# Optimization experiments

Hardware: AMD Instinct MI355X
Metric: run time of the kernel (lower is better)

## Reference

```python
import jax, jax.numpy as jnp
import numpy as np

# Production-scale dims (see shape_source)
B = 8            # batch size
P = 32768        # points per sample
Q = 2048         # supernodes per sample
N = B * P        # 262144 total points
S = B * Q        # 16384 total supernodes
MAX_DEG = 32
E = S * MAX_DEG  # 524288 edges
IN_DIM = 16
H = 192          # hidden_dim, divisible by ndim=3, per-dim 64 (even) -> no padding
NDIM = 3
MAX_WAVELENGTH = 10000.0


def sincos_embed(pos):
    # ContinuousSincosEmbed: dim split evenly over ndim, sin/cos halves per coord
    dpn = H // NDIM                                                   # 64
    omega = 1.0 / MAX_WAVELENGTH ** (jnp.arange(0, dpn, 2, dtype=jnp.float32) / dpn)  # [dpn/2]
    out = pos[..., None] * omega                                      # [N, ndim, dpn/2]
    emb = jnp.concatenate([jnp.sin(out), jnp.cos(out)], axis=-1)      # [N, ndim, dpn]
    return emb.reshape(pos.shape[0], H)                               # [N, H]


def setup_inputs() -> dict:
    key = jax.random.key(0)
    ks = jax.random.split(key, 8)
    input_feat = jax.random.normal(ks[0], (N, IN_DIM), jnp.float32)
    input_pos = jax.random.uniform(ks[1], (N, NDIM), jnp.float32) * 100.0
    batch_idx = jnp.repeat(jnp.arange(B, dtype=jnp.int32), P)
    # Q supernodes per sample, globally sorted & unique (as from radius_graph filter)
    ar = jnp.arange(S, dtype=jnp.int32)
    supernode_idxs = (ar // Q) * P + (ar % Q)
    # edges: each supernode is dst of MAX_DEG edges; src within same sample
    dst_idx = jnp.repeat(supernode_idxs, MAX_DEG)
    src_idx = (dst_idx // P) * P + jax.random.randint(ks[2], (E,), 0, P, dtype=jnp.int32)
    # params (LinearProjection = affine)
    W_in = jax.random.normal(ks[3], (IN_DIM, H), jnp.float32) / np.sqrt(IN_DIM)
    b_in = jnp.zeros((H,), jnp.float32)
    W1 = jax.random.normal(ks[4], (2 * H, H), jnp.float32) / np.sqrt(2 * H)
    b1 = jnp.zeros((H,), jnp.float32)
    W2 = jax.random.normal(ks[5], (H, H), jnp.float32) / np.sqrt(H)
    b2 = jnp.zeros((H,), jnp.float32)
    return {"input_feat": input_feat, "input_pos": input_pos,
            "supernode_idxs": supernode_idxs, "batch_idx": batch_idx,
            "src_idx": src_idx, "dst_idx": dst_idx,
            "W_in": W_in, "b_in": b_in, "W1": W1, "b1": b1, "W2": W2, "b2": b2}


def reference(input_feat, input_pos, supernode_idxs, batch_idx, src_idx, dst_idx,
              W_in, b_in, W1, b1, W2, b2):
    # x = input_proj(feat) + pos_embed(pos)        [N, H]
    x = input_feat @ W_in + b_in + sincos_embed(input_pos)
    # gather src/dst node features per edge, concat  [E, 2H]
    m = jnp.concatenate([x[src_idx], x[dst_idx]], axis=1)
    # message MLP: Linear -> GELU(exact) -> Linear   [E, H]
    m = jax.nn.gelu(m @ W1 + b1, approximate=False) @ W2 + b2
    # segment-mean by destination supernode (segment_csr 'mean' equivalent)
    seg = jnp.searchsorted(supernode_idxs, dst_idx)  # [E] in [0, S)
    sums = jax.ops.segment_sum(m, seg, num_segments=S)
    cnt = jax.ops.segment_sum(jnp.ones((E,), m.dtype), seg, num_segments=S)
    pooled = sums / cnt[:, None]                     # [S, H]
    return pooled.reshape(B, S // B, H)              # [B, Q, H]
```

## Files before the change

### kernel.cpp

```cpp
#include <hip/hip_runtime.h>
#include <hip/hip_bf16.h>


#define HD 192
#define INF 16
#define N_NODES 262144
#define N_SUP 16384
#define ROWB 384
#define EP_TILES 4

typedef __attribute__((ext_vector_type(8))) short bf16x8;
typedef __attribute__((ext_vector_type(4))) float f32x4;

__device__ __forceinline__ unsigned f2bf(float f) {
    unsigned x = __float_as_uint(f);
    return (x + 0x7fffu + ((x >> 16) & 1u)) >> 16;
}
__device__ __forceinline__ float bf2f(unsigned short u) {
    return __uint_as_float(((unsigned)u) << 16);
}
__device__ __forceinline__ void gload16(const void* g, void* l) {
    __builtin_amdgcn_global_load_lds(
        (const __attribute__((address_space(1))) unsigned int*)g,
        (__attribute__((address_space(3))) unsigned int*)l, 16, 0, 0);
}
__device__ __forceinline__ void gelu_acc(float v, float& acc) {
    const float m   = v * fmaf(v * v, -0.1029392f, -2.3021178f);
    const float den = 1.f + exp2f(m);
    const float r   = __builtin_amdgcn_rcpf(den);
    acc = fmaf(v, r, acc);
}

__global__ void prep_kernel(const float* __restrict__ W1,
                            const float* __restrict__ Win,
                            unsigned short* __restrict__ Wt,
                            unsigned short* __restrict__ Wb,
                            float* __restrict__ Wint)
{
    const int i = blockIdx.x * 256 + threadIdx.x;
    if (i < 36864) {
        const int n = i / HD, k = i % HD;
        Wt[i] = (unsigned short)f2bf(W1[k * HD + n]);
    } else if (i < 73728) {
        const int j = i - 36864;
        const int n = j / HD, k = j % HD;
        Wb[j] = (unsigned short)f2bf(W1[(size_t)(HD + k) * HD + n]);
    } else if (i < 76800) {
        const int j = i - 73728;
        const int c = j / INF, k = j % INF;
        Wint[j] = Win[k * HD + c];
    }
}

__global__ __launch_bounds__(256, 2)
void xcomp_kernel(const float* __restrict__ feat,
                  const float* __restrict__ pos,
                  const float* __restrict__ Wint,
                  const float* __restrict__ bin,
                  unsigned short* __restrict__ xswz)
{
    __shared__ __align__(16) float feat_s[4][256];
    __shared__ float pos_s[4][48];
    __shared__ __align__(16) unsigned short dstg[4][16 * HD];

    const int t = threadIdx.x, w = t >> 6, l = t & 63;

    float win[3][INF];
    #pragma unroll
    for (int d = 0; d < 3; ++d)
        #pragma unroll
        for (int q = 0; q < 4; ++q)
            *reinterpret_cast<float4*>(&win[d][q * 4]) =
                *reinterpret_cast<const float4*>(Wint + (size_t)(l + 64 * d) * INF + q * 4);
    float bcol[3];
    #pragma unroll
    for (int d = 0; d < 3; ++d) bcol[d] = bin[l + 64 * d];
    const float om = exp2f(-(float)(l & 31) * 0.41524101186098287f);
    const float phase = (l < 32) ? 0.f : 1.57079632679f;

    for (int gg = 0; gg < 4; ++gg) {
        const int row0 = blockIdx.x * 256 + gg * 64 + w * 16;

        {
            const float4 f4 = *reinterpret_cast<const float4*>(
                feat + (size_t)(row0 + (l >> 2)) * INF + (l & 3) * 4);
            *reinterpret_cast<float4*>(&feat_s[w][(l >> 2) * 16 + (l & 3) * 4]) = f4;
            if (l < 48) pos_s[w][l] = pos[(size_t)row0 * 3 + l];
        }

        for (int r = 0; r < 16; ++r) {
            float fr[INF];
            #pragma unroll
            for (int q = 0; q < 4; ++q)
                *reinterpret_cast<float4*>(&fr[q * 4]) =
                    *reinterpret_cast<const float4*>(&feat_s[w][r * 16 + q * 4]);
            #pragma unroll
            for (int d = 0; d < 3; ++d) {
                const float pe = __sinf(fmaf(pos_s[w][r * 3 + d], om, phase));
                float acc = bcol[d] + pe;
                #pragma unroll
                for (int k = 0; k < INF; ++k) acc = fmaf(fr[k], win[d][k], acc);
                dstg[w][r * HD + l + 64 * d] = (unsigned short)f2bf(acc);
            }
        }

        #pragma unroll
        for (int q = 0; q < 6; ++q) {
            const int id = q * 64 + l;
            const int rl = id / 24, c = id % 24;
            const bf16x8 v = *reinterpret_cast<const bf16x8*>(&dstg[w][rl * HD + c * 8]);
            *reinterpret_cast<bf16x8*>((char*)xswz +
                (size_t)(row0 + rl) * ROWB + ((c ^ (rl & 7)) * 16)) = v;
        }
    }
}

template<bool GATHER>
__global__ __launch_bounds__(256, 2)
void agemm_kernel(const unsigned short* __restrict__ xswz,
                  const int* __restrict__ gidx,
                  const unsigned short* __restrict__ Wt,
                  const float* __restrict__ bias,
                  unsigned short* __restrict__ outp,
                  const int out_stride,
                  const int ntiles)
{
    __shared__ __align__(16) unsigned short xbuf[2][64 * HD];
    __shared__ int nid[64];

    const int t = threadIdx.x, w = t >> 6, l = t & 63;

    bf16x8 bfr[3][6];
    #pragma unroll
    for (int ct = 0; ct < 3; ++ct) {
        const int col = w * 48 + ct * 16 + (l & 15);
        const unsigned short* wp = Wt + (size_t)col * HD + (l >> 4) * 8;
        #pragma unroll
        for (int ks = 0; ks < 6; ++ks)
            bfr[ct][ks] = *reinterpret_cast<const bf16x8*>(wp + ks * 32);
    }
    float bias_c[3] = {0.f, 0.f, 0.f};
    if (GATHER) {
        #pragma unroll
        for (int ct = 0; ct < 3; ++ct) bias_c[ct] = bias[w * 48 + ct * 16 + (l & 15)];
        if (t < 64) nid[t] = gidx[blockIdx.x * 64 + t];
        __syncthreads();
    }

    auto STAGE = [&](int tile, int buf) {
        char* lbase = (char*)&xbuf[buf][0];
        if constexpr (GATHER) {
            #pragma unroll
            for (int i = 0; i < 6; ++i) {
                const int slot = w * 64 + i * 256 + l;
                const int r = slot / 24, p = slot % 24;
                const int node = nid[r];
                const char* src = (const char*)xswz + (size_t)node * ROWB +
                                  (((p ^ (r & 7)) ^ (node & 7)) * 16);
                gload16(src, lbase + w * 1024 + i * 4096);
            }
        } else {
            const char* gb = (const char*)xswz +
                             (size_t)(blockIdx.x * ntiles + tile) * 64 * ROWB;
            #pragma unroll
            for (int i = 0; i < 6; ++i)
                gload16(gb + w * 1024 + i * 4096 + l * 16, lbase + w * 1024 + i * 4096);
        }
    };

    STAGE(0, 0);
    __syncthreads();

    for (int tt = 0; tt < ntiles; ++tt) {
        const int cur = tt & 1;
        if (tt + 1 < ntiles) STAGE(tt + 1, cur ^ 1);

        f32x4 acc[4][3];
        #pragma unroll
        for (int rt = 0; rt < 4; ++rt)
            #pragma unroll
            for (int ct = 0; ct < 3; ++ct)
                acc[rt][ct] = (f32x4){0.f, 0.f, 0.f, 0.f};

        const char* xb = (const char*)&xbuf[cur][0];
        #pragma unroll
        for (int ks = 0; ks < 6; ++ks) {
            bf16x8 af[4];
            #pragma unroll
            for (int rt = 0; rt < 4; ++rt) {
                const int row = rt * 16 + (l & 15);
                const int p = (ks * 4 + (l >> 4)) ^ (l & 7);
                af[rt] = *reinterpret_cast<const bf16x8*>(xb + row * ROWB + p * 16);
            }
            #pragma unroll
            for (int rt = 0; rt < 4; ++rt)
                #pragma unroll
                for (int ct = 0; ct < 3; ++ct)
                    acc[rt][ct] = __builtin_amdgcn_mfma_f32_16x16x32_bf16(
                        af[rt], bfr[ct][ks], acc[rt][ct], 0, 0, 0);
        }
        __syncthreads();

        char* db = (char*)&xbuf[cur][0];
        #pragma unroll
        for (int rt = 0; rt < 4; ++rt)
            #pragma unroll
            for (int ct = 0; ct < 3; ++ct) {
                const int col = w * 48 + ct * 16 + (l & 15);
                const int ch = col >> 3, off = col & 7;
                #pragma unroll
                for (int j = 0; j < 4; ++j) {
                    const int row = rt * 16 + (l >> 4) * 4 + j;
                    *reinterpret_cast<unsigned short*>(
                        db + row * ROWB + ((ch ^ (row & 7)) * 16) + off * 2) =
                        (unsigned short)f2bf(acc[rt][ct][j] + bias_c[ct]);
                }
            }
        const size_t orow0 = GATHER ? (size_t)blockIdx.x * 64
                                    : (size_t)(blockIdx.x * ntiles + tt) * 64;
        #pragma unroll
        for (int q = 0; q < 6; ++q) {
            const int id = q * 64 + l;
            const int rid = id / 6, cc = id % 6;
            const int c = w * 6 + cc;
            const bf16x8 v = *reinterpret_cast<const bf16x8*>(
                db + rid * ROWB + ((c ^ (rid & 7)) * 16));
            *reinterpret_cast<bf16x8*>(outp + (orow0 + rid) * out_stride + c * 8) = v;
        }
        __syncthreads();
    }
}

__global__ __launch_bounds__(256, 2)
void edgepool_kernel(const unsigned short* __restrict__ xswz,
                     const int* __restrict__ src_idx,
                     const unsigned short* __restrict__ Wt,
                     const unsigned short* __restrict__ bC,
                     float* __restrict__ g)
{
    __shared__ __align__(16) unsigned short xbuf[2][64 * HD];

    const int t = threadIdx.x, w = t >> 6, l = t & 63;

    bf16x8 bfr[3][6];
    #pragma unroll
    for (int ct = 0; ct < 3; ++ct) {
        const int col = w * 48 + ct * 16 + (l & 15);
        const unsigned short* wp = Wt + (size_t)col * HD + (l >> 4) * 8;
        #pragma unroll
        for (int ks = 0; ks < 6; ++ks)
            bfr[ct][ks] = *reinterpret_cast<const bf16x8*>(wp + ks * 32);
    }

    auto STAGE = [&](int tile, int buf) {
        char* lbase = (char*)&xbuf[buf][0] + w * 1024;
        const int* se = src_idx + (size_t)(blockIdx.x * EP_TILES + tile) * 64;
        #pragma unroll
        for (int i = 0; i < 6; ++i) {
            const int slot = w * 64 + i * 256 + l;
            const int r = slot / 24, p = slot % 24;
            const int node = se[r];
            const char* src = (const char*)xswz + (size_t)node * ROWB +
                              (((p ^ (r & 7)) ^ (node & 7)) * 16);
            gload16(src, lbase + i * 4096);
        }
    };

    STAGE(0, 0);
    __syncthreads();

    for (int tt = 0; tt < EP_TILES; ++tt) {
        const int cur = tt & 1;
        if (tt + 1 < EP_TILES) STAGE(tt + 1, cur ^ 1);

        f32x4 acc[4][3];
        #pragma unroll
        for (int rt = 0; rt < 4; ++rt)
            #pragma unroll
            for (int ct = 0; ct < 3; ++ct)
                acc[rt][ct] = (f32x4){0.f, 0.f, 0.f, 0.f};

        const char* xb = (const char*)&xbuf[cur][0];
        #pragma unroll
        for (int ks = 0; ks < 6; ++ks) {
            bf16x8 af[4];
            #pragma unroll
            for (int rt = 0; rt < 4; ++rt) {
                const int row = rt * 16 + (l & 15);
                const int p = (ks * 4 + (l >> 4)) ^ (l & 7);
                af[rt] = *reinterpret_cast<const bf16x8*>(xb + row * ROWB + p * 16);
            }
            #pragma unroll
            for (int rt = 0; rt < 4; ++rt)
                #pragma unroll
                for (int ct = 0; ct < 3; ++ct)
                    acc[rt][ct] = __builtin_amdgcn_mfma_f32_16x16x32_bf16(
                        af[rt], bfr[ct][ks], acc[rt][ct], 0, 0, 0);
        }

        const size_t s0 = (size_t)(blockIdx.x * EP_TILES + tt) * 2;
        float bval[2][3];
        #pragma unroll
        for (int sn = 0; sn < 2; ++sn)
            #pragma unroll
            for (int ct = 0; ct < 3; ++ct)
                bval[sn][ct] = bf2f(bC[(s0 + sn) * 384 + w * 48 + ct * 16 + (l & 15)]);

        __syncthreads();

        #pragma unroll
        for (int sn = 0; sn < 2; ++sn)
            #pragma unroll
            for (int ct = 0; ct < 3; ++ct) {
                float part = 0.f;
                #pragma unroll
                for (int rr = 0; rr < 2; ++rr)
                    #pragma unroll
                    for (int j = 0; j < 4; ++j)
                        gelu_acc(acc[sn * 2 + rr][ct][j] + bval[sn][ct], part);
                part += __shfl_xor(part, 16);
                part += __shfl_xor(part, 32);
                if (l < 16)
                    g[(s0 + sn) * HD + w * 48 + ct * 16 + l] = part * 0.03125f;
            }
    }
}

__global__ __launch_bounds__(256, 2)
void gemm192_kernel(const float* __restrict__ A,
                    const float* __restrict__ W,
                    const float* __restrict__ bias,
                    float* __restrict__ out)
{
    __shared__ float xsf[64][196];
    __shared__ float wchunk[32][HD];
    const int t    = threadIdx.x;
    const int row0 = blockIdx.x * 64;

    const float4* ap = reinterpret_cast<const float4*>(A + (size_t)row0 * HD);
    #pragma unroll
    for (int q = 0; q < 12; ++q) {
        const int f4 = t + q * 256;
        const int r = f4 / 48, c = f4 % 48;
        *reinterpret_cast<float4*>(&xsf[r][c * 4]) = ap[f4];
    }

    const int tr = t >> 4;
    const int tc = t & 15;
    float acc[4][12];
    #pragma unroll
    for (int i = 0; i < 4; ++i)
        #pragma unroll
        for (int j = 0; j < 12; ++j) acc[i][j] = 0.f;

    for (int kc = 0; kc < 6; ++kc) {
        __syncthreads();
        {
            const float4* wp = reinterpret_cast<const float4*>(W + kc * 32 * HD);
            float4* wsp = reinterpret_cast<float4*>(&wchunk[0][0]);
            #pragma unroll
            for (int q = 0; q < 6; ++q) wsp[t + q * 256] = wp[t + q * 256];
        }
        __syncthreads();
        #pragma unroll 4
        for (int k = 0; k < 32; ++k) {
            const int kg = kc * 32 + k;
            float xv[4];
            #pragma unroll
            for (int i = 0; i < 4; ++i) xv[i] = xsf[tr * 4 + i][kg];
            float wv[12];
            #pragma unroll
            for (int j4 = 0; j4 < 3; ++j4)
                *reinterpret_cast<float4*>(&wv[j4 * 4]) =
                    *reinterpret_cast<const float4*>(&wchunk[k][tc * 12 + j4 * 4]);
            #pragma unroll
            for (int i = 0; i < 4; ++i)
                #pragma unroll
                for (int j = 0; j < 12; ++j)
                    acc[i][j] = fmaf(xv[i], wv[j], acc[i][j]);
        }
    }

    float bb[12];
    #pragma unroll
    for (int j = 0; j < 12; ++j) bb[j] = bias[tc * 12 + j];

    #pragma unroll
    for (int i = 0; i < 4; ++i) {
        float* o = out + (size_t)(row0 + tr * 4 + i) * HD + tc * 12;
        #pragma unroll
        for (int j4 = 0; j4 < 3; ++j4) {
            float4 v;
            v.x = acc[i][j4 * 4 + 0] + bb[j4 * 4 + 0];
            v.y = acc[i][j4 * 4 + 1] + bb[j4 * 4 + 1];
            v.z = acc[i][j4 * 4 + 2] + bb[j4 * 4 + 2];
            v.w = acc[i][j4 * 4 + 3] + bb[j4 * 4 + 3];
            *reinterpret_cast<float4*>(o + j4 * 4) = v;
        }
    }
}

extern "C" void kernel_launch(void* const* d_in, const int* in_sizes, int n_in,
                              void* d_out, int out_size, void* d_ws, size_t ws_size,
                              hipStream_t stream)
{
    const float* feat = (const float*)d_in[0];
    const float* pos  = (const float*)d_in[1];
    const int*   sup  = (const int*)d_in[2];
    const int*   src  = (const int*)d_in[4];
    const float* Win  = (const float*)d_in[6];
    const float* bin  = (const float*)d_in[7];
    const float* W1   = (const float*)d_in[8];
    const float* b1   = (const float*)d_in[9];
    const float* W2   = (const float*)d_in[10];
    const float* b2   = (const float*)d_in[11];

    char* ws = (char*)d_ws;
    unsigned short* Wt   = (unsigned short*)ws;
    unsigned short* Wb   = (unsigned short*)(ws + 73728);
    float*          Wint = (float*)(ws + 147456);
    unsigned short* x    = (unsigned short*)(ws + 159744);
    char*           C    = ws + 159744 + 100663296;
    float* out = (float*)d_out;

    prep_kernel<<<300, 256, 0, stream>>>(W1, Win, Wt, Wb, Wint);
    xcomp_kernel<<<N_NODES / 256, 256, 0, stream>>>(feat, pos, Wint, bin, x);
    agemm_kernel<true><<<N_SUP / 64, 256, 0, stream>>>(
        x, sup, Wb, b1, (unsigned short*)C, 384, 1);
    edgepool_kernel<<<N_SUP / (2 * EP_TILES), 256, 0, stream>>>(
        x, src, Wt, (const unsigned short*)C, (float*)C);
    gemm192_kernel<<<N_SUP / 64, 256, 0, stream>>>((const float*)C, W2, b2, out);
}
```

Measured before the change: 248.9 us.

## Triple-buffer edge gather pipeline with explicit vmcnt waits and prefetched indices

The edgepool kernel moves to a three-stage LDS ring with prefetch distance two. It replaces __syncthreads with s_waitcnt vmcnt plus s_barrier, doubles tiles per block, and preloads src indices and bias rows into shared memory so tile loops avoid global index loads. The xcomp kernel software-prefetches the next group's feat/pos into registers and raises its occupancy hint. This should hide gather latency better, at the cost of more LDS per block, fewer blocks in the edge kernel, and fragile hand-counted vmcnt values.

```diff
diff --git a/kernel.cpp b/kernel.cpp
--- a/kernel.cpp
+++ b/kernel.cpp
@@ -7,7 +7,7 @@
 #define N_NODES 262144
 #define N_SUP 16384
 #define ROWB 384
-#define EP_TILES 4
+#define EP_TILES 8
 
 typedef __attribute__((ext_vector_type(8))) short bf16x8;
 typedef __attribute__((ext_vector_type(4))) float f32x4;
@@ -52,7 +52,7 @@
     }
 }
 
-__global__ __launch_bounds__(256, 2)
+__global__ __launch_bounds__(256, 3)
 void xcomp_kernel(const float* __restrict__ feat,
                   const float* __restrict__ pos,
                   const float* __restrict__ Wint,
@@ -78,14 +78,20 @@
     const float om = exp2f(-(float)(l & 31) * 0.41524101186098287f);
     const float phase = (l < 32) ? 0.f : 1.57079632679f;
 
+    int row0 = blockIdx.x * 256 + w * 16;
+    float4 fstage = *reinterpret_cast<const float4*>(
+        feat + (size_t)(row0 + (l >> 2)) * INF + (l & 3) * 4);
+    float pstage = (l < 48) ? pos[(size_t)row0 * 3 + l] : 0.f;
+
     for (int gg = 0; gg < 4; ++gg) {
-        const int row0 = blockIdx.x * 256 + gg * 64 + w * 16;
-
-        {
-            const float4 f4 = *reinterpret_cast<const float4*>(
-                feat + (size_t)(row0 + (l >> 2)) * INF + (l & 3) * 4);
-            *reinterpret_cast<float4*>(&feat_s[w][(l >> 2) * 16 + (l & 3) * 4]) = f4;
-            if (l < 48) pos_s[w][l] = pos[(size_t)row0 * 3 + l];
+        *reinterpret_cast<float4*>(&feat_s[w][(l >> 2) * 16 + (l & 3) * 4]) = fstage;
+        if (l < 48) pos_s[w][l] = pstage;
+
+        const int nrow0 = row0 + 64;
+        if (gg < 3) {
+            fstage = *reinterpret_cast<const float4*>(
+                feat + (size_t)(nrow0 + (l >> 2)) * INF + (l & 3) * 4);
+            if (l < 48) pstage = pos[(size_t)nrow0 * 3 + l];
         }
 
         for (int r = 0; r < 16; ++r) {
@@ -112,6 +118,7 @@
             *reinterpret_cast<bf16x8*>((char*)xswz +
                 (size_t)(row0 + rl) * ROWB + ((c ^ (rl & 7)) * 16)) = v;
         }
+        row0 = nrow0;
     }
 }
 
@@ -238,9 +245,25 @@
                      const unsigned short* __restrict__ bC,
                      float* __restrict__ g)
 {
-    __shared__ __align__(16) unsigned short xbuf[2][64 * HD];
+    __shared__ __align__(16) unsigned short xbuf[3][64 * HD];
+    __shared__ int sIdx[EP_TILES * 64];
+    __shared__ unsigned short bs[EP_TILES * 2 * HD];
 
     const int t = threadIdx.x, w = t >> 6, l = t & 63;
+
+    #pragma unroll
+    for (int i = 0; i < (EP_TILES * 64) / 256; ++i)
+        sIdx[t + i * 256] = src_idx[(size_t)blockIdx.x * (EP_TILES * 64) + t + i * 256];
+    {
+        const size_t srow0 = (size_t)blockIdx.x * (EP_TILES * 2);
+        #pragma unroll
+        for (int i = 0; i < 6; ++i) {
+            const int idx = t + i * 256;
+            const int r = idx / 96, c = idx % 96;
+            reinterpret_cast<unsigned*>(bs)[idx] =
+                *reinterpret_cast<const unsigned*>(bC + (srow0 + r) * 384 + c * 2);
+        }
+    }
 
     bf16x8 bfr[3][6];
     #pragma unroll
@@ -252,26 +275,38 @@
             bfr[ct][ks] = *reinterpret_cast<const bf16x8*>(wp + ks * 32);
     }
 
+    int rr[6], pp[6];
+    #pragma unroll
+    for (int i = 0; i < 6; ++i) {
+        const int slot = w * 64 + i * 256 + l;
+        rr[i] = slot / 24; pp[i] = slot % 24;
+    }
+
+    __syncthreads();
+
     auto STAGE = [&](int tile, int buf) {
         char* lbase = (char*)&xbuf[buf][0] + w * 1024;
-        const int* se = src_idx + (size_t)(blockIdx.x * EP_TILES + tile) * 64;
+        const int* se = &sIdx[tile * 64];
         #pragma unroll
         for (int i = 0; i < 6; ++i) {
-            const int slot = w * 64 + i * 256 + l;
-            const int r = slot / 24, p = slot % 24;
-            const int node = se[r];
+            const int node = se[rr[i]];
             const char* src = (const char*)xswz + (size_t)node * ROWB +
-                              (((p ^ (r & 7)) ^ (node & 7)) * 16);
+                              (((pp[i] ^ (rr[i] & 7)) ^ (node & 7)) * 16);
             gload16(src, lbase + i * 4096);
         }
     };
 
     STAGE(0, 0);
-    __syncthreads();
-
+    STAGE(1, 1);
+
+    #pragma unroll 1
     for (int tt = 0; tt < EP_TILES; ++tt) {
-        const int cur = tt & 1;
-        if (tt + 1 < EP_TILES) STAGE(tt + 1, cur ^ 1);
+        if (tt == 0) { asm volatile("s_waitcnt vmcnt(6)" ::: "memory"); }
+        else         { asm volatile("s_waitcnt vmcnt(12)" ::: "memory"); }
+        __builtin_amdgcn_s_barrier();
+        __builtin_amdgcn_sched_barrier(0);
+
+        if (tt + 2 < EP_TILES) STAGE(tt + 2, (tt + 2) % 3);
 
         f32x4 acc[4][3];
         #pragma unroll
@@ -280,7 +315,7 @@
             for (int ct = 0; ct < 3; ++ct)
                 acc[rt][ct] = (f32x4){0.f, 0.f, 0.f, 0.f};
 
-        const char* xb = (const char*)&xbuf[cur][0];
+        const char* xb = (const char*)&xbuf[tt % 3][0];
         #pragma unroll
         for (int ks = 0; ks < 6; ++ks) {
             bf16x8 af[4];
@@ -298,30 +333,23 @@
                         af[rt], bfr[ct][ks], acc[rt][ct], 0, 0, 0);
         }
 
-        const size_t s0 = (size_t)(blockIdx.x * EP_TILES + tt) * 2;
-        float bval[2][3];
+        const int s0l = tt * 2;
         #pragma unroll
         for (int sn = 0; sn < 2; ++sn)
             #pragma unroll
-            for (int ct = 0; ct < 3; ++ct)
-                bval[sn][ct] = bf2f(bC[(s0 + sn) * 384 + w * 48 + ct * 16 + (l & 15)]);
-
-        __syncthreads();
-
-        #pragma unroll
-        for (int sn = 0; sn < 2; ++sn)
-            #pragma unroll
             for (int ct = 0; ct < 3; ++ct) {
+                const float bval = bf2f(bs[(s0l + sn) * HD + w * 48 + ct * 16 + (l & 15)]);
                 float part = 0.f;
                 #pragma unroll
-                for (int rr = 0; rr < 2; ++rr)
+                for (int r2 = 0; r2 < 2; ++r2)
                     #pragma unroll
                     for (int j = 0; j < 4; ++j)
-                        gelu_acc(acc[sn * 2 + rr][ct][j] + bval[sn][ct], part);
+                        gelu_acc(acc[sn * 2 + r2][ct][j] + bval, part);
                 part += __shfl_xor(part, 16);
                 part += __shfl_xor(part, 32);
                 if (l < 16)
-                    g[(s0 + sn) * HD + w * 48 + ct * 16 + l] = part * 0.03125f;
+                    g[((size_t)blockIdx.x * (EP_TILES * 2) + s0l + sn) * HD +
+                      w * 48 + ct * 16 + l] = part * 0.03125f;
             }
     }
 }
```

New measurement: 260.9 us. 1.05x slower.
